# Kernel tuning notes

Hardware: AMD Instinct MI355X
Metric: run time of the kernel (lower is better)

## Reference

```python
import jax, jax.numpy as jnp
import numpy as np

B, S, VOCAB, P, K, R = 64, 512, 50000, 300, 50, 5


def setup_inputs() -> dict:
    key = jax.random.key(0)
    k0, k1, k2, k3, k4, k5, k6 = jax.random.split(key, 7)
    idx = jax.random.randint(k0, (B, S), 0, VOCAB)
    emb = jax.random.normal(k1, (VOCAB, P), dtype=jnp.float32) * 0.02
    emb = emb.at[0].set(0.0)  # padding_idx=0 row is zero
    C = jax.random.normal(k2, (K, P), dtype=jnp.float32)  # label embeddings ~ N(0,1)
    conv_w = jax.random.normal(k3, (1, 1, 1, 2 * R + 1), dtype=jnp.float32) * 0.1
    conv_b = jax.random.normal(k4, (1,), dtype=jnp.float32) * 0.1
    W2 = jax.random.normal(k5, (K, P), dtype=jnp.float32) / np.sqrt(P).astype(np.float32)
    b2 = jax.random.normal(k6, (K,), dtype=jnp.float32) * 0.01
    return {"idx": idx, "emb": emb, "C": C, "conv_w": conv_w, "conv_b": conv_b, "W2": W2, "b2": b2}


def reference(idx, emb, C, conv_w, conv_b, W2, b2):
    # Embed sentence: [B, S, P]
    x = emb[idx]
    # Cosine label attention
    x_hat = x / (jnp.linalg.norm(x, axis=2, keepdims=True) + 0.001)
    l_hat = C / (jnp.linalg.norm(C, axis=1, keepdims=True) + 0.001)
    G_hat = jnp.einsum('kp,bsp->bks', l_hat, x_hat)  # [B, K, S]
    # Pad seq dim by R on both sides, then conv2d(1->1, kernel (1, 2R+1))
    G_pad = jnp.pad(G_hat, ((0, 0), (0, 0), (R, R)))
    m = jax.lax.conv_general_dilated(
        G_pad[:, None, :, :], conv_w, window_strides=(1, 1), padding='VALID',
        dimension_numbers=('NCHW', 'OIHW', 'NCHW'))[:, 0] + conv_b[0]  # [B, K, S]
    m = jax.nn.relu(m)
    m = jnp.max(m, axis=1)  # max over labels -> [B, S]
    beta = jax.nn.softmax(m, axis=1)[..., None]  # [B, S, 1]
    pooled = jnp.mean(beta * x, axis=1)  # [B, P]
    # Dropout is identity in eval mode; final linear P -> K
    return pooled @ W2.T + b2
```

## Files before the change

kernel.cpp:

```cpp
#include <hip/hip_runtime.h>

#define B_   64
#define S_   512
#define P_   300
#define K_   50
#define MPAD 64
#define LDX  344

typedef short short8v __attribute__((ext_vector_type(8)));
typedef float float4v __attribute__((ext_vector_type(4)));

__device__ __forceinline__ short f2bf(float f) {
  unsigned u = __builtin_bit_cast(unsigned, f);
  u = (u + 0x7FFFu + ((u >> 16) & 1u)) >> 16;
  return (short)u;
}

__global__ __launch_bounds__(64) void k1_prep(const float* __restrict__ C,
                                              const float* __restrict__ W2,
                                              short* __restrict__ apack) {
  int bid = blockIdx.x;
  int mat = bid / 40;
  int rem = bid - mat * 40;
  int mt  = rem / 10;
  int ks  = rem - mt * 10;
  int lane = threadIdx.x;
  __shared__ float invn[16];
  if (mat == 0) {
    int rl = lane >> 2, q = lane & 3;
    int m = mt * 16 + rl;
    float ss = 0.f;
    if (m < K_) {
      for (int p = q; p < P_; p += 4) { float v = C[m * P_ + p]; ss += v * v; }
    }
    ss += __shfl_xor(ss, 1);
    ss += __shfl_xor(ss, 2);
    if (q == 0) invn[rl] = 1.f / (sqrtf(ss) + 0.001f);
  }
  __syncthreads();
  int ml = lane & 15, quad = lane >> 4;
  int m = mt * 16 + ml;
  const float* src = (mat == 0) ? C : W2;
  short8v v8;
  #pragma unroll
  for (int j = 0; j < 8; ++j) {
    int k = ks * 32 + quad * 8 + j;
    float v = 0.f;
    if (m < K_ && k < P_) {
      v = src[m * P_ + k];
      if (mat == 0) v *= invn[ml];
    }
    v8[j] = f2bf(v);
  }
  *(short8v*)(apack + (size_t)(((mat * 4 + mt) * 10 + ks) * 512 + lane * 8)) = v8;
}

__global__ __launch_bounds__(256) void k2_gemm(const int* __restrict__ idx,
                                               const float* __restrict__ emb,
                                               const short* __restrict__ apack,
                                               float* __restrict__ G,
                                               float* __restrict__ Yt) {
  __shared__ __align__(16) short xt[64][LDX];
  __shared__ float scale_s[64];
  int bid = blockIdx.x;
  int b = bid >> 3, s0 = (bid & 7) * 64;
  int tid = threadIdx.x;
  int w = tid >> 6, lane = tid & 63;

  for (int r = 0; r < 16; ++r) {
    int ls = w * 16 + r;
    int row = idx[b * S_ + s0 + ls];
    const float4* src = (const float4*)(emb + (size_t)row * P_);
    float4 v = src[lane];
    float ss = v.x * v.x + v.y * v.y + v.z * v.z + v.w * v.w;
    short4 h; h.x = f2bf(v.x); h.y = f2bf(v.y); h.z = f2bf(v.z); h.w = f2bf(v.w);
    *(short4*)&xt[ls][4 * lane] = h;
    if (lane < 11) {
      float4 v2 = src[64 + lane];
      ss += v2.x * v2.x + v2.y * v2.y + v2.z * v2.z + v2.w * v2.w;
      short4 h2; h2.x = f2bf(v2.x); h2.y = f2bf(v2.y); h2.z = f2bf(v2.z); h2.w = f2bf(v2.w);
      *(short4*)&xt[ls][256 + 4 * lane] = h2;
    } else if (lane < 16) {
      short4 z = {0, 0, 0, 0};
      *(short4*)&xt[ls][300 + 4 * (lane - 11)] = z;
    }
    #pragma unroll
    for (int off = 32; off > 0; off >>= 1) ss += __shfl_xor(ss, off);
    if (lane == 0) scale_s[ls] = 1.f / (sqrtf(ss) + 0.001f);
  }
  __syncthreads();

  float4v accG[4] = {}, accY[4] = {};
  int ml = lane & 15, quad = lane >> 4;
  const short8v* a1p = (const short8v*)(apack) + (size_t)((0 * 4 + w) * 10) * 64 + lane;
  const short8v* a2p = (const short8v*)(apack) + (size_t)((1 * 4 + w) * 10) * 64 + lane;
  #pragma unroll
  for (int ks = 0; ks < 10; ++ks) {
    short8v a1 = a1p[ks * 64];
    short8v a2 = a2p[ks * 64];
    int kk = ks * 32 + quad * 8;
    #pragma unroll
    for (int nt = 0; nt < 4; ++nt) {
      short8v bf = *(const short8v*)&xt[nt * 16 + ml][kk];
      accG[nt] = __builtin_amdgcn_mfma_f32_16x16x32_bf16(a1, bf, accG[nt], 0, 0, 0);
      accY[nt] = __builtin_amdgcn_mfma_f32_16x16x32_bf16(a2, bf, accY[nt], 0, 0, 0);
    }
  }

  #pragma unroll
  for (int nt = 0; nt < 4; ++nt) {
    int sl = nt * 16 + ml;
    float sc = scale_s[sl];
    int sg = s0 + sl;
    #pragma unroll
    for (int reg = 0; reg < 4; ++reg) {
      int m = w * 16 + quad * 4 + reg;
      G [(size_t)(b * MPAD + m) * S_ + sg] = accG[nt][reg] * sc;
      Yt[(size_t)(b * MPAD + m) * S_ + sg] = accY[nt][reg];
    }
  }
}

__global__ __launch_bounds__(256) void k3a_conv(const float* __restrict__ G,
                                                const float* __restrict__ conv_w,
                                                const float* __restrict__ conv_b,
                                                float* __restrict__ mbuf) {
  __shared__ float gt[K_][76];
  __shared__ float mpart[4][64];
  int bid = blockIdx.x;
  int b = bid >> 3, s0 = (bid & 7) * 64;
  int tid = threadIdx.x;
  for (int e = tid; e < K_ * 74; e += 256) {
    int k = e / 74, i = e - k * 74;
    int s = s0 - 5 + i;
    gt[k][i] = (s >= 0 && s < S_) ? G[(size_t)(b * MPAD + k) * S_ + s] : 0.f;
  }
  float wv[11];
  #pragma unroll
  for (int t = 0; t < 11; ++t) wv[t] = conv_w[t];
  float cb = conv_b[0];
  __syncthreads();
  int sl = tid & 63, kg = tid >> 6;
  float mx = 0.f;
  for (int k = kg; k < K_; k += 4) {
    float acc = cb;
    #pragma unroll
    for (int t = 0; t < 11; ++t) acc += wv[t] * gt[k][sl + t];
    mx = fmaxf(mx, fmaxf(acc, 0.f));
  }
  mpart[kg][sl] = mx;
  __syncthreads();
  if (tid < 64) {
    float m0 = fmaxf(fmaxf(mpart[0][tid], mpart[1][tid]),
                     fmaxf(mpart[2][tid], mpart[3][tid]));
    mbuf[b * S_ + s0 + tid] = m0;
  }
}

__global__ __launch_bounds__(512) void k3b_out(const float* __restrict__ mbuf,
                                               const float* __restrict__ Yt,
                                               const float* __restrict__ b2,
                                               float* __restrict__ out) {
  __shared__ float beta[S_];
  __shared__ float redm[8];
  __shared__ float reds[8];
  int b = blockIdx.x;
  int tid = threadIdx.x;
  int lane = tid & 63, wv = tid >> 6;
  float mv = mbuf[b * S_ + tid];
  float r = mv;
  #pragma unroll
  for (int off = 32; off > 0; off >>= 1) r = fmaxf(r, __shfl_xor(r, off));
  if (lane == 0) redm[wv] = r;
  __syncthreads();
  float bm = redm[0];
  #pragma unroll
  for (int i = 1; i < 8; ++i) bm = fmaxf(bm, redm[i]);
  float e = __expf(mv - bm);
  r = e;
  #pragma unroll
  for (int off = 32; off > 0; off >>= 1) r += __shfl_xor(r, off);
  if (lane == 0) reds[wv] = r;
  __syncthreads();
  float sum = 0.f;
  #pragma unroll
  for (int i = 0; i < 8; ++i) sum += reds[i];
  beta[tid] = e / (sum * (float)S_);
  __syncthreads();
  for (int k = wv; k < K_; k += 8) {
    const float* yrow = Yt + (size_t)(b * MPAD + k) * S_;
    float acc = 0.f;
    #pragma unroll
    for (int i = 0; i < 8; ++i) {
      int s = lane + i * 64;
      acc += beta[s] * yrow[s];
    }
    #pragma unroll
    for (int off = 32; off > 0; off >>= 1) acc += __shfl_xor(acc, off);
    if (lane == 0) out[b * K_ + k] = acc + b2[k];
  }
}

extern "C" void kernel_launch(void* const* d_in, const int* in_sizes, int n_in,
                              void* d_out, int out_size, void* d_ws, size_t ws_size,
                              hipStream_t stream) {
  const int*   idx    = (const int*)  d_in[0];
  const float* emb    = (const float*)d_in[1];
  const float* C      = (const float*)d_in[2];
  const float* conv_w = (const float*)d_in[3];
  const float* conv_b = (const float*)d_in[4];
  const float* W2     = (const float*)d_in[5];
  const float* b2     = (const float*)d_in[6];
  float* out = (float*)d_out;

  char* ws = (char*)d_ws;
  short* apack = (short*)(ws);
  float* G     = (float*)(ws + 81920);
  float* Yt    = (float*)(ws + 81920 + 8388608);
  float* mbuf  = (float*)(ws + 81920 + 2 * 8388608);

  hipLaunchKernelGGL(k1_prep, dim3(80),  dim3(64),  0, stream, C, W2, apack);
  hipLaunchKernelGGL(k2_gemm, dim3(512), dim3(256), 0, stream, idx, emb, apack, G, Yt);
  hipLaunchKernelGGL(k3a_conv, dim3(512), dim3(256), 0, stream, G, conv_w, conv_b, mbuf);
  hipLaunchKernelGGL(k3b_out, dim3(64),  dim3(512), 0, stream, mbuf, Yt, b2, out);
}
```

Before: 159.3 us.

## Store G/Y intermediates as bf16 and fuse conv and output kernels

Intermediate G and Y tensors are now written as bf16 instead of fp32, and only rows with m<K are stored. The conv/max kernel and the softmax/pooling kernel are merged into one per-batch kernel that keeps the whole G row in shared memory, which drops the mbuf round trip and one launch. The gather loop is also split so the 16 norm reductions run after all loads are issued. In exchange, the fused kernel runs only 64 blocks, so less of the GPU is in use for the conv stage, and bf16 storage of G and Y adds rounding error.

```diff
diff --git a/kernel.cpp b/kernel.cpp
--- a/kernel.cpp
+++ b/kernel.cpp
@@ -6,6 +6,7 @@
 #define K_   50
 #define MPAD 64
 #define LDX  344
+#define LDG  528
 
 typedef short short8v __attribute__((ext_vector_type(8)));
 typedef float float4v __attribute__((ext_vector_type(4)));
@@ -14,6 +15,9 @@
   unsigned u = __builtin_bit_cast(unsigned, f);
   u = (u + 0x7FFFu + ((u >> 16) & 1u)) >> 16;
   return (short)u;
+}
+__device__ __forceinline__ float bf2f(short h) {
+  return __builtin_bit_cast(float, ((unsigned)(unsigned short)h) << 16);
 }
 
 __global__ __launch_bounds__(64) void k1_prep(const float* __restrict__ C,
@@ -58,8 +62,8 @@
 __global__ __launch_bounds__(256) void k2_gemm(const int* __restrict__ idx,
                                                const float* __restrict__ emb,
                                                const short* __restrict__ apack,
-                                               float* __restrict__ G,
-                                               float* __restrict__ Yt) {
+                                               short* __restrict__ G,
+                                               short* __restrict__ Yt) {
   __shared__ __align__(16) short xt[64][LDX];
   __shared__ float scale_s[64];
   int bid = blockIdx.x;
@@ -67,6 +71,8 @@
   int tid = threadIdx.x;
   int w = tid >> 6, lane = tid & 63;
 
+  float ssr[16];
+  #pragma unroll
   for (int r = 0; r < 16; ++r) {
     int ls = w * 16 + r;
     int row = idx[b * S_ + s0 + ls];
@@ -84,9 +90,14 @@
       short4 z = {0, 0, 0, 0};
       *(short4*)&xt[ls][300 + 4 * (lane - 11)] = z;
     }
+    ssr[r] = ss;
+  }
+  #pragma unroll
+  for (int r = 0; r < 16; ++r) {
+    float ss = ssr[r];
     #pragma unroll
     for (int off = 32; off > 0; off >>= 1) ss += __shfl_xor(ss, off);
-    if (lane == 0) scale_s[ls] = 1.f / (sqrtf(ss) + 0.001f);
+    if (lane == 0) scale_s[w * 16 + r] = 1.f / (sqrtf(ss) + 0.001f);
   }
   __syncthreads();
 
@@ -115,86 +126,79 @@
     #pragma unroll
     for (int reg = 0; reg < 4; ++reg) {
       int m = w * 16 + quad * 4 + reg;
-      G [(size_t)(b * MPAD + m) * S_ + sg] = accG[nt][reg] * sc;
-      Yt[(size_t)(b * MPAD + m) * S_ + sg] = accY[nt][reg];
-    }
-  }
-}
-
-__global__ __launch_bounds__(256) void k3a_conv(const float* __restrict__ G,
+      if (m < K_) {
+        G [(size_t)(b * MPAD + m) * S_ + sg] = f2bf(accG[nt][reg] * sc);
+        Yt[(size_t)(b * MPAD + m) * S_ + sg] = f2bf(accY[nt][reg]);
+      }
+    }
+  }
+}
+
+__global__ __launch_bounds__(512) void k3_fused(const short* __restrict__ G,
                                                 const float* __restrict__ conv_w,
                                                 const float* __restrict__ conv_b,
-                                                float* __restrict__ mbuf) {
-  __shared__ float gt[K_][76];
-  __shared__ float mpart[4][64];
-  int bid = blockIdx.x;
-  int b = bid >> 3, s0 = (bid & 7) * 64;
-  int tid = threadIdx.x;
-  for (int e = tid; e < K_ * 74; e += 256) {
-    int k = e / 74, i = e - k * 74;
-    int s = s0 - 5 + i;
-    gt[k][i] = (s >= 0 && s < S_) ? G[(size_t)(b * MPAD + k) * S_ + s] : 0.f;
-  }
-  float wv[11];
-  #pragma unroll
-  for (int t = 0; t < 11; ++t) wv[t] = conv_w[t];
-  float cb = conv_b[0];
-  __syncthreads();
-  int sl = tid & 63, kg = tid >> 6;
-  float mx = 0.f;
-  for (int k = kg; k < K_; k += 4) {
-    float acc = cb;
-    #pragma unroll
-    for (int t = 0; t < 11; ++t) acc += wv[t] * gt[k][sl + t];
-    mx = fmaxf(mx, fmaxf(acc, 0.f));
-  }
-  mpart[kg][sl] = mx;
-  __syncthreads();
-  if (tid < 64) {
-    float m0 = fmaxf(fmaxf(mpart[0][tid], mpart[1][tid]),
-                     fmaxf(mpart[2][tid], mpart[3][tid]));
-    mbuf[b * S_ + s0 + tid] = m0;
-  }
-}
-
-__global__ __launch_bounds__(512) void k3b_out(const float* __restrict__ mbuf,
-                                               const float* __restrict__ Yt,
-                                               const float* __restrict__ b2,
-                                               float* __restrict__ out) {
+                                                const short* __restrict__ Yt,
+                                                const float* __restrict__ b2,
+                                                float* __restrict__ out) {
+  __shared__ __align__(16) short gt[K_][LDG];
   __shared__ float beta[S_];
-  __shared__ float redm[8];
-  __shared__ float reds[8];
+  __shared__ float red[8];
   int b = blockIdx.x;
   int tid = threadIdx.x;
   int lane = tid & 63, wv = tid >> 6;
-  float mv = mbuf[b * S_ + tid];
-  float r = mv;
+
+  for (int e = tid; e < K_ * 8; e += 512) {
+    int k = e >> 3, j = e & 7;
+    gt[k][j] = 0;
+    gt[k][520 + j] = 0;
+  }
+  for (int k = wv; k < K_; k += 8) {
+    short8v v = *(const short8v*)(G + (((size_t)(b * MPAD + k)) << 9) + lane * 8);
+    *(short8v*)&gt[k][8 + lane * 8] = v;
+  }
+  float wvv[11];
+  #pragma unroll
+  for (int t = 0; t < 11; ++t) wvv[t] = conv_w[t];
+  float cb = conv_b[0];
+  __syncthreads();
+
+  float mx = 0.f;
+  for (int k = 0; k < K_; ++k) {
+    float acc = cb;
+    #pragma unroll
+    for (int t = 0; t < 11; ++t) acc += wvv[t] * bf2f(gt[k][3 + tid + t]);
+    mx = fmaxf(mx, fmaxf(acc, 0.f));
+  }
+
+  float r = mx;
   #pragma unroll
   for (int off = 32; off > 0; off >>= 1) r = fmaxf(r, __shfl_xor(r, off));
-  if (lane == 0) redm[wv] = r;
-  __syncthreads();
-  float bm = redm[0];
-  #pragma unroll
-  for (int i = 1; i < 8; ++i) bm = fmaxf(bm, redm[i]);
-  float e = __expf(mv - bm);
+  if (lane == 0) red[wv] = r;
+  __syncthreads();
+  float bm = red[0];
+  #pragma unroll
+  for (int i = 1; i < 8; ++i) bm = fmaxf(bm, red[i]);
+  float e = __expf(mx - bm);
   r = e;
   #pragma unroll
   for (int off = 32; off > 0; off >>= 1) r += __shfl_xor(r, off);
-  if (lane == 0) reds[wv] = r;
+  __syncthreads();
+  if (lane == 0) red[wv] = r;
   __syncthreads();
   float sum = 0.f;
   #pragma unroll
-  for (int i = 0; i < 8; ++i) sum += reds[i];
+  for (int i = 0; i < 8; ++i) sum += red[i];
   beta[tid] = e / (sum * (float)S_);
   __syncthreads();
+
   for (int k = wv; k < K_; k += 8) {
-    const float* yrow = Yt + (size_t)(b * MPAD + k) * S_;
-    float acc = 0.f;
-    #pragma unroll
-    for (int i = 0; i < 8; ++i) {
-      int s = lane + i * 64;
-      acc += beta[s] * yrow[s];
-    }
+    short8v y = *(const short8v*)(Yt + (((size_t)(b * MPAD + k)) << 9) + lane * 8);
+    const float4* bp = (const float4*)&beta[lane * 8];
+    float4 b0 = bp[0], b1 = bp[1];
+    float acc = b0.x * bf2f(y[0]) + b0.y * bf2f(y[1]) +
+                b0.z * bf2f(y[2]) + b0.w * bf2f(y[3]) +
+                b1.x * bf2f(y[4]) + b1.y * bf2f(y[5]) +
+                b1.z * bf2f(y[6]) + b1.w * bf2f(y[7]);
     #pragma unroll
     for (int off = 32; off > 0; off >>= 1) acc += __shfl_xor(acc, off);
     if (lane == 0) out[b * K_ + k] = acc + b2[k];
@@ -215,12 +219,10 @@
 
   char* ws = (char*)d_ws;
   short* apack = (short*)(ws);
-  float* G     = (float*)(ws + 81920);
-  float* Yt    = (float*)(ws + 81920 + 8388608);
-  float* mbuf  = (float*)(ws + 81920 + 2 * 8388608);
-
-  hipLaunchKernelGGL(k1_prep, dim3(80),  dim3(64),  0, stream, C, W2, apack);
-  hipLaunchKernelGGL(k2_gemm, dim3(512), dim3(256), 0, stream, idx, emb, apack, G, Yt);
-  hipLaunchKernelGGL(k3a_conv, dim3(512), dim3(256), 0, stream, G, conv_w, conv_b, mbuf);
-  hipLaunchKernelGGL(k3b_out, dim3(64),  dim3(512), 0, stream, mbuf, Yt, b2, out);
-}
+  short* G     = (short*)(ws + 81920);
+  short* Yt    = (short*)(ws + 81920 + 4194304);
+
+  hipLaunchKernelGGL(k1_prep,  dim3(80),  dim3(64),  0, stream, C, W2, apack);
+  hipLaunchKernelGGL(k2_gemm,  dim3(512), dim3(256), 0, stream, idx, emb, apack, G, Yt);
+  hipLaunchKernelGGL(k3_fused, dim3(64),  dim3(512), 0, stream, G, conv_w, conv_b, Yt, b2, out);
+}
```

Measured after the change: 165.0 us. 1.04x slower.
